# Kernel tuning notes

Hardware: AMD Instinct MI355X
Metric: run time of the kernel (lower is better)

The kernel has to match this reference:

```python
import jax, jax.numpy as jnp
import numpy as np

SIZES = (1, 2, 4, 8)
C_IN = 64
KC = C_IN // 8      # key_channels = out_channels // 8 = 8
VC = C_IN           # value_channels = out_channels = 64
N_STAGES = len(SIZES)


def setup_inputs() -> dict:
    key = jax.random.key(0)
    ks = jax.random.split(key, 16)
    N, C, H, W = 1, C_IN, 64, 64
    inp = {
        "x1": jax.random.normal(ks[0], (N, C, H, W), jnp.float32),
        "x2": jax.random.normal(ks[1], (N, C, H, W), jnp.float32),
        # per-stage 1x1 conv weights (stacked over the 4 PAM stages)
        "Wq": jax.random.normal(ks[2], (N_STAGES, KC, C), jnp.float32) * 0.02,
        "bq": jnp.zeros((N_STAGES, KC), jnp.float32),
        "gammaq": 1.0 + jax.random.normal(ks[3], (N_STAGES, KC), jnp.float32) * 0.02,
        "betaq": jnp.zeros((N_STAGES, KC), jnp.float32),
        "Wk": jax.random.normal(ks[4], (N_STAGES, KC, C), jnp.float32) * 0.02,
        "bk": jnp.zeros((N_STAGES, KC), jnp.float32),
        "gammak": 1.0 + jax.random.normal(ks[5], (N_STAGES, KC), jnp.float32) * 0.02,
        "betak": jnp.zeros((N_STAGES, KC), jnp.float32),
        "Wv": jax.random.normal(ks[6], (N_STAGES, VC, C), jnp.float32) * 0.02,
        "bv": jnp.zeros((N_STAGES, VC), jnp.float32),
        # final 1x1 conv: in = C * n_stages, out = C, no bias
        "Wo": jax.random.normal(ks[7], (C, VC * N_STAGES), jnp.float32) * 0.02,
    }
    return inp


def _pam_block(x, Wq, bq, gq, betq, Wk, bk, gk, betk, Wv, bv, scale):
    # x: [N, C, H, 2W] (two images concatenated along width)
    N, C, H, W2 = x.shape
    w = W2 // 2
    kc = Wq.shape[0]

    def proj(W, b):  # 1x1 conv
        return jnp.einsum('nchw,kc->nkhw', x, W) + b[:, None, None]

    # BatchNorm (inference form: zero running mean / unit variance) folded to affine
    q = gq[:, None, None] * proj(Wq, bq) + betq[:, None, None]
    k = gk[:, None, None] * proj(Wk, bk) + betk[:, None, None]
    v = proj(Wv, bv)

    hl, wl = H // scale, w // scale

    def to_blocks(t):
        ch = t.shape[1]
        # stack left/right halves on a trailing axis: [N, ch, H, w, 2]
        t = jnp.stack([t[..., :w], t[..., w:]], axis=-1)
        # split into scale x scale spatial blocks -> [N, s*s, ch, hl*wl*2]
        t = t.reshape(N, ch, scale, hl, scale, wl, 2)
        t = t.transpose(0, 2, 4, 1, 3, 5, 6)
        return t.reshape(N, scale * scale, ch, hl * wl * 2)

    qb, kb, vb = to_blocks(q), to_blocks(k), to_blocks(v)

    sim = jnp.einsum('nbkp,nbkq->nbpq', qb, kb) * (kc ** -0.5)
    att = jax.nn.softmax(sim, axis=-1)
    # context = V @ att^T : ctx[c,p] = sum_q v[c,q] * att[p,q]
    ctx = jnp.einsum('nbcq,nbpq->nbcp', vb, att)

    Cv = Wv.shape[0]
    ctx = ctx.reshape(N, scale, scale, Cv, hl, wl, 2)
    ctx = ctx.transpose(0, 3, 1, 4, 2, 5, 6).reshape(N, Cv, H, w, 2)
    # re-concatenate the two halves along width -> [N, Cv, H, 2w]
    return jnp.concatenate([ctx[..., 0], ctx[..., 1]], axis=3)


def reference(x1, x2, Wq, bq, gammaq, betaq, Wk, bk, gammak, betak, Wv, bv, Wo):
    h_w = x1.shape[3]
    x = jnp.concatenate([x1, x2], axis=3)  # [N, C, H, 2W]
    priors = [
        _pam_block(x, Wq[i], bq[i], gammaq[i], betaq[i],
                   Wk[i], bk[i], gammak[i], betak[i],
                   Wv[i], bv[i], SIZES[i])
        for i in range(N_STAGES)
    ]
    cat = jnp.concatenate(priors, axis=1)  # [N, 4C, H, 2W]
    out = jnp.einsum('ndhw,od->nohw', cat, Wo)  # final 1x1 conv, no bias
    return out[:, :, :, :h_w], out[:, :, :, h_w:]


if __name__ == '__main__':
    o1, o2 = reference(**setup_inputs())
    print(o1.shape, o2.shape)
```

## Files before the change

### kernel.cpp

```cpp
#include <hip/hip_runtime.h>


typedef _Float16 f16x8 __attribute__((ext_vector_type(8)));
typedef float f32x16 __attribute__((ext_vector_type(16)));
typedef short bf16x8 __attribute__((ext_vector_type(8)));

__device__ __forceinline__ unsigned short f2bf(float f){
    union{float f;unsigned int i;}v; v.f=f;
    unsigned int r = v.i + 0x7fffu + ((v.i>>16)&1u);
    return (unsigned short)(r>>16);
}
__device__ __forceinline__ unsigned short f2h(float f){
    union{_Float16 h; unsigned short u;}v; v.h = (_Float16)f; return v.u;
}
__device__ __forceinline__ unsigned pack2h(float a, float b){
    auto pk = __builtin_amdgcn_cvt_pkrtz(a, b);
    unsigned u; __builtin_memcpy(&u, &pk, 4); return u;
}
__device__ __forceinline__ float exp2fast(float x){ return __builtin_amdgcn_exp2f(x); }
__device__ __forceinline__ int rfl(int x){ return __builtin_amdgcn_readfirstlane(x); }

#define QMUL 0.5100697233f

__global__ __launch_bounds__(256) void proj_all_kernel(
    const float* __restrict__ x1, const float* __restrict__ x2,
    const float* __restrict__ Wq, const float* __restrict__ bq,
    const float* __restrict__ gq, const float* __restrict__ beq,
    const float* __restrict__ Wk, const float* __restrict__ bk,
    const float* __restrict__ gk, const float* __restrict__ bek,
    const float* __restrict__ Wv, const float* __restrict__ bv,
    unsigned short* __restrict__ Qb, unsigned short* __restrict__ Kb,
    unsigned short* __restrict__ Vf)
{
    __shared__ __align__(16) float xs[64][68];
    __shared__ __align__(16) unsigned vqk[64][8];
    __shared__ __align__(16) unsigned short vv[64][64];

    const int wg = blockIdx.x, st = wg >> 8, rr = wg & 255;
    const int chunk = rr >> 1, cgrp = rr & 1;
    const int lgP = 13 - 2*st, Pm1 = (1<<lgP) - 1;
    const int hb = 6 - st, wlm = (1<<hb) - 1;
    const int t = threadIdx.x;
    const int gp0 = chunk*64;
    const int blk = gp0 >> lgP, p0 = gp0 & Pm1;
    const int si = blk >> st, sj = blk & ((1<<st)-1);
    const int hwbase = ((si<<hb)<<6) | (sj<<hb);

    for (int idx = t; idx < 4096; idx += 256) {
        int c = idx >> 6, g = idx & 63;
        int p = p0 + g, half = p & 1, pw = p >> 1;
        int hw = hwbase | ((pw>>hb)<<6) | (pw & wlm);
        xs[g][c] = (half ? x2 : x1)[c*4096 + hw];
    }
    __syncthreads();

    const int px = t & 63, wv = t >> 6;
    float xr[64];
    #pragma unroll
    for (int q4 = 0; q4 < 16; ++q4)
        *(float4*)&xr[q4*4] = *(const float4*)&xs[px][q4*4];

#define VRANGE(LO,HI)                                              \
    for (int ch = (LO); ch < (HI); ++ch) {                         \
        const int cu = rfl(st*64 + ch);                            \
        const float* wp = Wv + cu*64;                              \
        float d = bv[cu];                                          \
        _Pragma("unroll")                                          \
        for (int k = 0; k < 64; ++k) d += wp[k]*xr[k];             \
        vv[ch][px] = f2h(d);                                       \
    }
#define KPROJ(CH,DST)                                              \
    {   const int cu = rfl(st*8 + (CH));                           \
        const float* wp = Wk + cu*64;                              \
        float d = 0.f;                                             \
        _Pragma("unroll")                                          \
        for (int k = 0; k < 64; ++k) d += wp[k]*xr[k];             \
        float gm = gk[cu];                                         \
        (DST) = gm*(d + bk[cu]) + bek[cu]; }

    if (cgrp == 0) {
        if (wv == 0) {
            float qv8[8];
            for (int ch = 0; ch < 8; ++ch) {
                const int cu = rfl(st*8 + ch);
                const float* wp = Wq + cu*64;
                float d = 0.f;
                #pragma unroll
                for (int k = 0; k < 64; ++k) d += wp[k]*xr[k];
                float gm = gq[cu];
                qv8[ch] = (gm*(d + bq[cu]) + beq[cu])*QMUL;
            }
            #pragma unroll
            for (int i = 0; i < 4; ++i) vqk[px][i] = pack2h(qv8[2*i], qv8[2*i+1]);
            float k0v, k1v; KPROJ(0, k0v) KPROJ(1, k1v)
            vqk[px][4] = pack2h(k0v, k1v);
        } else if (wv == 1) {
            float ka, kb2;
            KPROJ(2, ka) KPROJ(3, kb2) vqk[px][5] = pack2h(ka, kb2);
            KPROJ(4, ka) KPROJ(5, kb2) vqk[px][6] = pack2h(ka, kb2);
            KPROJ(6, ka) KPROJ(7, kb2) vqk[px][7] = pack2h(ka, kb2);
            VRANGE(0, 4)
        } else if (wv == 2) { VRANGE(4, 14) }
        else               { VRANGE(14, 24) }
    } else {
        if      (wv == 0) { VRANGE(24, 34) }
        else if (wv == 1) { VRANGE(34, 44) }
        else if (wv == 2) { VRANGE(44, 54) }
        else              { VRANGE(54, 64) }
    }
#undef VRANGE
#undef KPROJ
    __syncthreads();

    unsigned short* Vst = Vf + st*524288 + (blk << (lgP+6));
    if (cgrp == 0) {
        if (t < 64) {
            *(uint4*)(Qb + st*65536 + (gp0 + t)*8) = *(const uint4*)&vqk[t][0];
        } else if (t < 128) {
            int p2 = t - 64;
            *(uint4*)(Kb + st*65536 + (gp0 + p2)*8) = *(const uint4*)&vqk[p2][4];
        }
        if (t < 192) {
            int ch = t >> 3, q = t & 7;
            int kb = q >> 1, lhi = q & 1;
            unsigned short tmp[8];
            #pragma unroll
            for (int u = 0; u < 8; ++u) {
                int s = q*8 + u;
                tmp[u] = vv[ch][((s&1)<<5) | (s>>1)];
            }
            *(uint4*)(Vst + p0*64 + kb*1024 + (lhi*32 + ch)*8) = *(const uint4*)tmp;
        }
    } else {
        for (int task = t; task < 320; task += 256) {
            int ch = 24 + (task >> 3), q = task & 7;
            int kb = q >> 1, lhi = q & 1;
            int b = (ch >= 32) ? 1 : 0, l31 = ch & 31;
            unsigned short tmp[8];
            #pragma unroll
            for (int u = 0; u < 8; ++u) {
                int s = q*8 + u;
                tmp[u] = vv[ch][((s&1)<<5) | (s>>1)];
            }
            *(uint4*)(Vst + p0*64 + kb*1024 + b*512 + (lhi*32 + l31)*8) = *(const uint4*)tmp;
        }
    }
}

__global__ __launch_bounds__(512) void attn_kernel(
    const unsigned short* __restrict__ Qb, const unsigned short* __restrict__ Kb,
    const unsigned short* __restrict__ Vf,
    float* __restrict__ PART, float* __restrict__ LPART)
{
    __shared__ __align__(16) float BB[8192];
    __shared__ float Lm[128];
    __shared__ float SCm[8][64];

    const int wg = blockIdx.x;
    const int t = threadIdx.x, lane = t & 63, wv = t >> 6;
    const int l31 = lane & 31, lhi = lane >> 5;

    int st, qt, slot, kbase, nkw;
    if (wg < 512)       { st=0; qt=wg>>1;  slot=wg&1;
                          kbase=(wg&1)*4096 + wv*512; nkw=512; }
    else if (wg < 1024) { int r=wg-512;  st=1; qt=r>>1; slot=2+(r&1);
                          kbase=(r&1)*1024 + wv*128;  nkw=128; }
    else if (wg < 1280) { st=2; qt=wg-1024; slot=4; kbase=wv*64; nkw=64; }
    else                { st=3; qt=wg-1280; slot=5; kbase=wv*64;
                          nkw=(wv<2)?64:0; }

    const int lgP = 13 - 2*st, P = 1 << lgP;
    const int blk = qt >> (lgP - 5);
    const int q0  = (qt & ((P>>5)-1)) * 32;

    const unsigned short* Qg = Qb + st*65536 + blk*P*8;
    const unsigned short* Kg = Kb + st*65536 + blk*P*8;
    const unsigned short* Vg = Vf + st*524288 + blk*P*64;

    f16x8 qb = *(const f16x8*)(Qg + (q0 + l31)*8);

    f32x16 acc0, acc1;
    #pragma unroll
    for (int r = 0; r < 16; ++r) { acc0[r] = 0.f; acc1[r] = 0.f; }
    float rs[4];
    #pragma unroll
    for (int r = 0; r < 4; ++r) rs[r] = 0.f;

    for (int k0 = kbase; k0 < kbase + nkw; k0 += 64) {
        f16x8 ka0, ka1;
        #pragma unroll
        for (int j = 0; j < 8; ++j) { ka0[j] = (_Float16)0.f; ka1[j] = (_Float16)0.f; }
        if (lane < 32) {
            ka0 = *(const f16x8*)(Kg + (k0 + l31)*8);
            ka1 = *(const f16x8*)(Kg + (k0 + 32 + l31)*8);
        }
        f32x16 S0, S1;
        #pragma unroll
        for (int r = 0; r < 16; ++r) { S0[r] = 0.f; S1[r] = 0.f; }
        S0 = __builtin_amdgcn_mfma_f32_32x32x16_f16(ka0, qb, S0, 0, 0, 0);
        S1 = __builtin_amdgcn_mfma_f32_32x32x16_f16(ka1, qb, S1, 0, 0, 0);

        unsigned pw[16];
        #pragma unroll
        for (int r = 0; r < 16; ++r) {
            float e0 = exp2fast(S0[r]);
            float e1 = exp2fast(S1[r]);
            rs[r & 3] += e0 + e1;
            pw[r] = pack2h(e0, e1);
        }

        #pragma unroll
        for (int kc = 0; kc < 4; ++kc) {
            f16x8 pb;
            __builtin_memcpy(&pb, &pw[kc*4], 16);
            const unsigned short* vbase = Vg + (k0 + kc*16)*64;
            f16x8 vb0 = *(const f16x8*)(vbase + lane*8);
            f16x8 vb1 = *(const f16x8*)(vbase + 512 + lane*8);
            acc0 = __builtin_amdgcn_mfma_f32_32x32x16_f16(pb, vb0, acc0, 0, 0, 0);
            acc1 = __builtin_amdgcn_mfma_f32_32x32x16_f16(pb, vb1, acc1, 0, 0, 0);
        }
    }

    float lsum = rs[0] + rs[1] + rs[2] + rs[3];
    SCm[wv][lhi*32 + l31] = lsum;
    __syncthreads();
    float lsum_reg = 0.f;
    if (lane < 32) lsum_reg = SCm[wv][l31] + SCm[wv][32 + l31];

    if (wv < 4) {
        float* B = BB + wv*2048;
        #pragma unroll
        for (int r = 0; r < 16; ++r) {
            int qrow = (r&3) + 8*(r>>2) + 4*lhi;
            B[qrow*64 + l31]      = acc0[r];
            B[qrow*64 + 32 + l31] = acc1[r];
        }
        if (lane < 32) Lm[wv*32 + l31] = lsum_reg;
    }
    __syncthreads();
    if (wv >= 4) {
        float* B = BB + (wv-4)*2048;
        #pragma unroll
        for (int r = 0; r < 16; ++r) {
            int qrow = (r&3) + 8*(r>>2) + 4*lhi;
            B[qrow*64 + l31]      += acc0[r];
            B[qrow*64 + 32 + l31] += acc1[r];
        }
        if (lane < 32) Lm[(wv-4)*32 + l31] += lsum_reg;
    }
    __syncthreads();

    float4* Pslab4 = (float4*)(PART + slot*524288 + qt*2048);
    const float4* B4 = (const float4*)BB;
    {
        float4 a = B4[t], b = B4[t+512], c = B4[t+1024], d = B4[t+1536];
        Pslab4[t] = float4{a.x+b.x+c.x+d.x, a.y+b.y+c.y+d.y,
                           a.z+b.z+c.z+d.z, a.w+b.w+c.w+d.w};
    }
    if (t < 32)
        LPART[slot*8192 + qt*32 + t] = Lm[t] + Lm[32+t] + Lm[64+t] + Lm[96+t];
}

__global__ __launch_bounds__(256) void normconv_kernel(
    const float* __restrict__ PART, const float* __restrict__ LPART,
    const float* __restrict__ Wo, float* __restrict__ out)
{
    __shared__ __align__(16) unsigned short csb[32][264];
    __shared__ __align__(16) unsigned short wof[16384];
    __shared__ float voutf[64][33];
    __shared__ float linv[4][32];
    __shared__ int gpar[4][32];
    const int t = threadIdx.x;
    const int px0 = blockIdx.x * 32;

    {
        int oc = t >> 2, d0 = (t & 3) * 64;
        for (int b = 0; b < 8; ++b) {
            int d = d0 + b*8;
            float4 w0 = *(const float4*)(Wo + oc*256 + d);
            float4 w1 = *(const float4*)(Wo + oc*256 + d + 4);
            unsigned short tmp[8];
            tmp[0]=f2bf(w0.x); tmp[1]=f2bf(w0.y); tmp[2]=f2bf(w0.z); tmp[3]=f2bf(w0.w);
            tmp[4]=f2bf(w1.x); tmp[5]=f2bf(w1.y); tmp[6]=f2bf(w1.z); tmp[7]=f2bf(w1.w);
            *(uint4*)&wof[(d>>3)*512 + oc*8] = *(const uint4*)tmp;
        }
    }
    if (t < 128) {
        const int s0tab[4] = {0,2,4,5};
        const int sctab[4] = {2,2,1,1};
        int stt = t >> 5, i = t & 31;
        int pix = px0 + i;
        int half = pix >> 12, hw = pix & 4095;
        int h = hw >> 6, w = hw & 63;
        int hb = 6 - stt, wlm = (1<<hb)-1;
        int si = h >> hb, sj = w >> hb, hi = h & wlm, wi = w & wlm;
        int blk = (si << stt) | sj;
        int p = (((hi << hb) | wi) << 1) | half;
        int gp = blk*(8192>>(2*stt)) + p;
        gpar[stt][i] = gp;
        int s0 = s0tab[stt];
        float l = LPART[s0*8192 + gp];
        if (sctab[stt] == 2) l += LPART[(s0+1)*8192 + gp];
        linv[stt][i] = 1.f / l;
    }
    __syncthreads();

    {
        const int s0tab[4] = {0,2,4,5};
        int gpx = t >> 3, cvg = (t & 7) * 8;
        for (int stt = 0; stt < 4; ++stt) {
            int gp = gpar[stt][gpx];
            const float* p = PART + s0tab[stt]*524288
                           + (gp>>5)*2048 + (gp&31)*64 + cvg;
            float4 a = *(const float4*)p;
            float4 b = *(const float4*)(p + 4);
            if (stt < 2) {
                float4 a2 = *(const float4*)(p + 524288);
                float4 b2 = *(const float4*)(p + 524288 + 4);
                a.x+=a2.x; a.y+=a2.y; a.z+=a2.z; a.w+=a2.w;
                b.x+=b2.x; b.y+=b2.y; b.z+=b2.z; b.w+=b2.w;
            }
            float li = linv[stt][gpx];
            unsigned short tmp[8];
            tmp[0]=f2bf(a.x*li); tmp[1]=f2bf(a.y*li); tmp[2]=f2bf(a.z*li); tmp[3]=f2bf(a.w*li);
            tmp[4]=f2bf(b.x*li); tmp[5]=f2bf(b.y*li); tmp[6]=f2bf(b.z*li); tmp[7]=f2bf(b.w*li);
            *(uint4*)&csb[gpx][stt*64 + cvg] = *(const uint4*)tmp;
        }
    }
    __syncthreads();

    const int lane = t & 63, wvv = t >> 6;
    const int l31 = lane & 31, lhi = lane >> 5;
    const int nh = wvv & 1, kh = wvv >> 1;
    f32x16 acc;
    #pragma unroll
    for (int r = 0; r < 16; ++r) acc[r] = 0.f;
    #pragma unroll
    for (int s = 0; s < 8; ++s) {
        int dg = kh*16 + s*2 + lhi;
        bf16x8 a = *(const bf16x8*)&csb[l31][kh*128 + s*16 + 8*lhi];
        bf16x8 b = *(const bf16x8*)&wof[dg*512 + (nh*32 + l31)*8];
        acc = __builtin_amdgcn_mfma_f32_32x32x16_bf16(a, b, acc, 0, 0, 0);
    }
    if (kh == 0) {
        #pragma unroll
        for (int r = 0; r < 16; ++r)
            voutf[nh*32 + l31][(r&3) + 8*(r>>2) + 4*lhi] = acc[r];
    }
    __syncthreads();
    if (kh == 1) {
        #pragma unroll
        for (int r = 0; r < 16; ++r)
            voutf[nh*32 + l31][(r&3) + 8*(r>>2) + 4*lhi] += acc[r];
    }
    __syncthreads();

    const int half = px0 >> 12, hw0 = px0 & 4095;
    float* obase = out + half*262144 + hw0;
    #pragma unroll
    for (int r = 0; r < 8; ++r) {
        int idx = t + r*256;
        int oc = idx >> 5, pxi = idx & 31;
        obase[oc*4096 + pxi] = voutf[oc][pxi];
    }
}

extern "C" void kernel_launch(void* const* d_in, const int* in_sizes, int n_in,
                              void* d_out, int out_size, void* d_ws, size_t ws_size,
                              hipStream_t stream)
{
    (void)out_size; (void)ws_size;
    const float *x1, *x2, *Wq, *bq, *gq, *beq, *Wk, *bk, *gk, *bek, *Wv, *bv, *Wo;

    if (n_in >= 13 && in_sizes[0] == 2048) {
        Wk  = (const float*)d_in[0];  Wo  = (const float*)d_in[1];
        Wq  = (const float*)d_in[2];  Wv  = (const float*)d_in[3];
        bek = (const float*)d_in[4];  beq = (const float*)d_in[5];
        bk  = (const float*)d_in[6];  bq  = (const float*)d_in[7];
        bv  = (const float*)d_in[8];  gk  = (const float*)d_in[9];
        gq  = (const float*)d_in[10];
        x1  = (const float*)d_in[11]; x2  = (const float*)d_in[12];
    } else {
        x1  = (const float*)d_in[0];  x2  = (const float*)d_in[1];
        Wq  = (const float*)d_in[2];  bq  = (const float*)d_in[3];
        gq  = (const float*)d_in[4];  beq = (const float*)d_in[5];
        Wk  = (const float*)d_in[6];  bk  = (const float*)d_in[7];
        gk  = (const float*)d_in[8];  bek = (const float*)d_in[9];
        Wv  = (const float*)d_in[10]; bv  = (const float*)d_in[11];
        Wo  = (const float*)d_in[12];
    }

    unsigned short* Qb = (unsigned short*)d_ws;
    unsigned short* Kb = Qb + 262144;
    unsigned short* Vf = Kb + 262144;
    float* PART  = (float*)d_ws + 1310720;
    float* LPART = PART + 3145728;

    proj_all_kernel<<<1024, 256, 0, stream>>>(x1,x2,Wq,bq,gq,beq,Wk,bk,gk,bek,Wv,bv,Qb,Kb,Vf);
    attn_kernel<<<1536, 512, 0, stream>>>(Qb,Kb,Vf,PART,LPART);
    normconv_kernel<<<256, 256, 0, stream>>>(PART, LPART, Wo, (float*)d_out);
}
```

Before: 132.4 us.

## Process two query tiles per attention wave to reuse K/V loads

The attention kernel now has each wave handle two 32-row query tiles against the same K and V fragments. Each K/V load feeds twice as many MFMAs, and the launch shrinks to half the blocks with 4 waves each. The projection dot products are also split into four independent accumulators to shorten the FMA dependency chain. In exchange, register pressure roughly doubles for the accumulators, occupancy and parallelism drop, and the epilogue runs twice with extra barriers.

```diff
diff --git a/kernel.cpp b/kernel.cpp
--- a/kernel.cpp
+++ b/kernel.cpp
@@ -21,6 +21,17 @@
 __device__ __forceinline__ int rfl(int x){ return __builtin_amdgcn_readfirstlane(x); }
 
 #define QMUL 0.5100697233f
+
+#define DOT64(WPTR, OUT) {                                         \
+    float a0=0.f, a1=0.f, a2=0.f, a3=0.f;                          \
+    _Pragma("unroll")                                              \
+    for (int k = 0; k < 16; ++k) {                                 \
+        a0 += (WPTR)[k]     * xr[k];                               \
+        a1 += (WPTR)[k+16]  * xr[k+16];                            \
+        a2 += (WPTR)[k+32]  * xr[k+32];                            \
+        a3 += (WPTR)[k+48]  * xr[k+48];                            \
+    }                                                              \
+    (OUT) = (a0+a1)+(a2+a3); }
 
 __global__ __launch_bounds__(256) void proj_all_kernel(
     const float* __restrict__ x1, const float* __restrict__ x2,
@@ -64,17 +75,13 @@
     for (int ch = (LO); ch < (HI); ++ch) {                         \
         const int cu = rfl(st*64 + ch);                            \
         const float* wp = Wv + cu*64;                              \
-        float d = bv[cu];                                          \
-        _Pragma("unroll")                                          \
-        for (int k = 0; k < 64; ++k) d += wp[k]*xr[k];             \
-        vv[ch][px] = f2h(d);                                       \
+        float d; DOT64(wp, d)                                      \
+        vv[ch][px] = f2h(d + bv[cu]);                              \
     }
 #define KPROJ(CH,DST)                                              \
     {   const int cu = rfl(st*8 + (CH));                           \
         const float* wp = Wk + cu*64;                              \
-        float d = 0.f;                                             \
-        _Pragma("unroll")                                          \
-        for (int k = 0; k < 64; ++k) d += wp[k]*xr[k];             \
+        float d; DOT64(wp, d)                                      \
         float gm = gk[cu];                                         \
         (DST) = gm*(d + bk[cu]) + bek[cu]; }
 
@@ -84,9 +91,7 @@
             for (int ch = 0; ch < 8; ++ch) {
                 const int cu = rfl(st*8 + ch);
                 const float* wp = Wq + cu*64;
-                float d = 0.f;
-                #pragma unroll
-                for (int k = 0; k < 64; ++k) d += wp[k]*xr[k];
+                float d; DOT64(wp, d)
                 float gm = gq[cu];
                 qv8[ch] = (gm*(d + bq[cu]) + beq[cu])*QMUL;
             }
@@ -147,118 +152,133 @@
     }
 }
 
-__global__ __launch_bounds__(512) void attn_kernel(
+__global__ __launch_bounds__(256) void attn_kernel(
     const unsigned short* __restrict__ Qb, const unsigned short* __restrict__ Kb,
     const unsigned short* __restrict__ Vf,
     float* __restrict__ PART, float* __restrict__ LPART)
 {
-    __shared__ __align__(16) float BB[8192];
-    __shared__ float Lm[128];
-    __shared__ float SCm[8][64];
+    __shared__ __align__(16) float BB[4096];
+    __shared__ float Lm[64];
+    __shared__ float SCm[4][64];
 
     const int wg = blockIdx.x;
     const int t = threadIdx.x, lane = t & 63, wv = t >> 6;
     const int l31 = lane & 31, lhi = lane >> 5;
 
-    int st, qt, slot, kbase, nkw;
-    if (wg < 512)       { st=0; qt=wg>>1;  slot=wg&1;
-                          kbase=(wg&1)*4096 + wv*512; nkw=512; }
-    else if (wg < 1024) { int r=wg-512;  st=1; qt=r>>1; slot=2+(r&1);
-                          kbase=(r&1)*1024 + wv*128;  nkw=128; }
-    else if (wg < 1280) { st=2; qt=wg-1024; slot=4; kbase=wv*64; nkw=64; }
-    else                { st=3; qt=wg-1280; slot=5; kbase=wv*64;
+    int st, u, slot, kbase, nkw;
+    if (wg < 256)       { st=0; u=wg>>1;        slot=wg&1;
+                          kbase=(wg&1)*4096 + wv*1024; nkw=1024; }
+    else if (wg < 512)  { int r=wg-256; st=1; u=r>>1; slot=2+(r&1);
+                          kbase=(r&1)*1024 + wv*256;  nkw=256; }
+    else if (wg < 640)  { st=2; u=wg-512; slot=4; kbase=wv*128; nkw=128; }
+    else                { st=3; u=wg-640; slot=5; kbase=wv*64;
                           nkw=(wv<2)?64:0; }
 
+    const int qtA = 2*u, qtB = 2*u+1;
     const int lgP = 13 - 2*st, P = 1 << lgP;
-    const int blk = qt >> (lgP - 5);
-    const int q0  = (qt & ((P>>5)-1)) * 32;
+    const int blk = qtA >> (lgP - 5);
+    const int q0  = (qtA & ((P>>5)-1)) * 32;
 
     const unsigned short* Qg = Qb + st*65536 + blk*P*8;
     const unsigned short* Kg = Kb + st*65536 + blk*P*8;
     const unsigned short* Vg = Vf + st*524288 + blk*P*64;
 
-    f16x8 qb = *(const f16x8*)(Qg + (q0 + l31)*8);
-
-    f32x16 acc0, acc1;
+    f16x8 qbA = *(const f16x8*)(Qg + (q0 + l31)*8);
+    f16x8 qbB = *(const f16x8*)(Qg + (q0 + 32 + l31)*8);
+
+    f32x16 accA0, accA1, accB0, accB1;
     #pragma unroll
-    for (int r = 0; r < 16; ++r) { acc0[r] = 0.f; acc1[r] = 0.f; }
-    float rs[4];
-    #pragma unroll
-    for (int r = 0; r < 4; ++r) rs[r] = 0.f;
+    for (int r = 0; r < 16; ++r) {
+        accA0[r]=0.f; accA1[r]=0.f; accB0[r]=0.f; accB1[r]=0.f;
+    }
+    float rsA[4] = {0.f,0.f,0.f,0.f}, rsB[4] = {0.f,0.f,0.f,0.f};
 
     for (int k0 = kbase; k0 < kbase + nkw; k0 += 64) {
         f16x8 ka0, ka1;
         #pragma unroll
-        for (int j = 0; j < 8; ++j) { ka0[j] = (_Float16)0.f; ka1[j] = (_Float16)0.f; }
+        for (int j = 0; j < 8; ++j) { ka0[j]=(_Float16)0.f; ka1[j]=(_Float16)0.f; }
         if (lane < 32) {
             ka0 = *(const f16x8*)(Kg + (k0 + l31)*8);
             ka1 = *(const f16x8*)(Kg + (k0 + 32 + l31)*8);
         }
-        f32x16 S0, S1;
-        #pragma unroll
-        for (int r = 0; r < 16; ++r) { S0[r] = 0.f; S1[r] = 0.f; }
-        S0 = __builtin_amdgcn_mfma_f32_32x32x16_f16(ka0, qb, S0, 0, 0, 0);
-        S1 = __builtin_amdgcn_mfma_f32_32x32x16_f16(ka1, qb, S1, 0, 0, 0);
-
-        unsigned pw[16];
+        f32x16 SA0, SA1, SB0, SB1;
+        #pragma unroll
+        for (int r = 0; r < 16; ++r) { SA0[r]=0.f; SA1[r]=0.f; SB0[r]=0.f; SB1[r]=0.f; }
+        SA0 = __builtin_amdgcn_mfma_f32_32x32x16_f16(ka0, qbA, SA0, 0, 0, 0);
+        SA1 = __builtin_amdgcn_mfma_f32_32x32x16_f16(ka1, qbA, SA1, 0, 0, 0);
+        SB0 = __builtin_amdgcn_mfma_f32_32x32x16_f16(ka0, qbB, SB0, 0, 0, 0);
+        SB1 = __builtin_amdgcn_mfma_f32_32x32x16_f16(ka1, qbB, SB1, 0, 0, 0);
+
+        unsigned pwA[16], pwB[16];
         #pragma unroll
         for (int r = 0; r < 16; ++r) {
-            float e0 = exp2fast(S0[r]);
-            float e1 = exp2fast(S1[r]);
-            rs[r & 3] += e0 + e1;
-            pw[r] = pack2h(e0, e1);
+            float a0 = exp2fast(SA0[r]), a1 = exp2fast(SA1[r]);
+            rsA[r & 3] += a0 + a1;  pwA[r] = pack2h(a0, a1);
+            float b0 = exp2fast(SB0[r]), b1 = exp2fast(SB1[r]);
+            rsB[r & 3] += b0 + b1;  pwB[r] = pack2h(b0, b1);
         }
 
         #pragma unroll
         for (int kc = 0; kc < 4; ++kc) {
-            f16x8 pb;
-            __builtin_memcpy(&pb, &pw[kc*4], 16);
+            f16x8 pbA, pbB;
+            __builtin_memcpy(&pbA, &pwA[kc*4], 16);
+            __builtin_memcpy(&pbB, &pwB[kc*4], 16);
             const unsigned short* vbase = Vg + (k0 + kc*16)*64;
             f16x8 vb0 = *(const f16x8*)(vbase + lane*8);
             f16x8 vb1 = *(const f16x8*)(vbase + 512 + lane*8);
-            acc0 = __builtin_amdgcn_mfma_f32_32x32x16_f16(pb, vb0, acc0, 0, 0, 0);
-            acc1 = __builtin_amdgcn_mfma_f32_32x32x16_f16(pb, vb1, acc1, 0, 0, 0);
-        }
-    }
-
-    float lsum = rs[0] + rs[1] + rs[2] + rs[3];
-    SCm[wv][lhi*32 + l31] = lsum;
-    __syncthreads();
-    float lsum_reg = 0.f;
-    if (lane < 32) lsum_reg = SCm[wv][l31] + SCm[wv][32 + l31];
-
-    if (wv < 4) {
-        float* B = BB + wv*2048;
-        #pragma unroll
-        for (int r = 0; r < 16; ++r) {
-            int qrow = (r&3) + 8*(r>>2) + 4*lhi;
-            B[qrow*64 + l31]      = acc0[r];
-            B[qrow*64 + 32 + l31] = acc1[r];
-        }
-        if (lane < 32) Lm[wv*32 + l31] = lsum_reg;
-    }
-    __syncthreads();
-    if (wv >= 4) {
-        float* B = BB + (wv-4)*2048;
-        #pragma unroll
-        for (int r = 0; r < 16; ++r) {
-            int qrow = (r&3) + 8*(r>>2) + 4*lhi;
-            B[qrow*64 + l31]      += acc0[r];
-            B[qrow*64 + 32 + l31] += acc1[r];
-        }
-        if (lane < 32) Lm[(wv-4)*32 + l31] += lsum_reg;
-    }
-    __syncthreads();
-
-    float4* Pslab4 = (float4*)(PART + slot*524288 + qt*2048);
-    const float4* B4 = (const float4*)BB;
-    {
-        float4 a = B4[t], b = B4[t+512], c = B4[t+1024], d = B4[t+1536];
-        Pslab4[t] = float4{a.x+b.x+c.x+d.x, a.y+b.y+c.y+d.y,
-                           a.z+b.z+c.z+d.z, a.w+b.w+c.w+d.w};
-    }
-    if (t < 32)
-        LPART[slot*8192 + qt*32 + t] = Lm[t] + Lm[32+t] + Lm[64+t] + Lm[96+t];
+            accA0 = __builtin_amdgcn_mfma_f32_32x32x16_f16(pbA, vb0, accA0, 0, 0, 0);
+            accA1 = __builtin_amdgcn_mfma_f32_32x32x16_f16(pbA, vb1, accA1, 0, 0, 0);
+            accB0 = __builtin_amdgcn_mfma_f32_32x32x16_f16(pbB, vb0, accB0, 0, 0, 0);
+            accB1 = __builtin_amdgcn_mfma_f32_32x32x16_f16(pbB, vb1, accB1, 0, 0, 0);
+        }
+    }
+
+#define EPILOGUE(ACC0, ACC1, RS, QT)                                    \
+    {                                                                   \
+        float lsum = (RS)[0]+(RS)[1]+(RS)[2]+(RS)[3];                   \
+        SCm[wv][lhi*32 + l31] = lsum;                                   \
+        __syncthreads();                                                \
+        float lrow = 0.f;                                               \
+        if (lane < 32) lrow = SCm[wv][l31] + SCm[wv][32 + l31];         \
+        if (wv == 0 || wv == 2) {                                       \
+            float* B = BB + (wv>>1)*2048;                               \
+            _Pragma("unroll")                                           \
+            for (int r = 0; r < 16; ++r) {                              \
+                int qrow = (r&3) + 8*(r>>2) + 4*lhi;                    \
+                B[qrow*64 + l31]      = (ACC0)[r];                      \
+                B[qrow*64 + 32 + l31] = (ACC1)[r];                      \
+            }                                                           \
+            if (lane < 32) Lm[(wv>>1)*32 + l31] = lrow;                 \
+        }                                                               \
+        __syncthreads();                                                \
+        if (wv == 1 || wv == 3) {                                       \
+            float* B = BB + (wv>>1)*2048;                               \
+            _Pragma("unroll")                                           \
+            for (int r = 0; r < 16; ++r) {                              \
+                int qrow = (r&3) + 8*(r>>2) + 4*lhi;                    \
+                B[qrow*64 + l31]      += (ACC0)[r];                     \
+                B[qrow*64 + 32 + l31] += (ACC1)[r];                     \
+            }                                                           \
+            if (lane < 32) Lm[(wv>>1)*32 + l31] += lrow;                \
+        }                                                               \
+        __syncthreads();                                                \
+        {                                                               \
+            float4* Pslab4 = (float4*)(PART + slot*524288 + (QT)*2048); \
+            const float4* B4 = (const float4*)BB;                       \
+            _Pragma("unroll")                                           \
+            for (int r = 0; r < 2; ++r) {                               \
+                int idx = t + r*256;                                    \
+                float4 a = B4[idx], b = B4[idx + 512];                  \
+                Pslab4[idx] = float4{a.x+b.x, a.y+b.y, a.z+b.z, a.w+b.w}; \
+            }                                                           \
+            if (t < 32) LPART[slot*8192 + (QT)*32 + t] = Lm[t] + Lm[32+t]; \
+        }                                                               \
+        __syncthreads();                                                \
+    }
+
+    EPILOGUE(accA0, accA1, rsA, qtA)
+    EPILOGUE(accB0, accB1, rsB, qtB)
+#undef EPILOGUE
 }
 
 __global__ __launch_bounds__(256) void normconv_kernel(
@@ -397,6 +417,6 @@
     float* LPART = PART + 3145728;
 
     proj_all_kernel<<<1024, 256, 0, stream>>>(x1,x2,Wq,bq,gq,beq,Wk,bk,gk,bek,Wv,bv,Qb,Kb,Vf);
-    attn_kernel<<<1536, 512, 0, stream>>>(Qb,Kb,Vf,PART,LPART);
+    attn_kernel<<<768, 256, 0, stream>>>(Qb,Kb,Vf,PART,LPART);
     normconv_kernel<<<256, 256, 0, stream>>>(PART, LPART, Wo, (float*)d_out);
 }
```

Measured after the change: 148.7 us. +12.3%, slower.
